# Performance work log

Measured on AMD Instinct MI355X. Metric: run time of the kernel, lower is better.

Reference implementation:

```python
import jax, jax.numpy as jnp
import numpy as np
from jax import lax

DG = 8  # deformable groups


def conv3(x, w, b):
    # 3x3 stride-1 SAME conv, NCHW/OIHW
    y = lax.conv_general_dilated(x, w, (1, 1), 'SAME',
                                 dimension_numbers=('NCHW', 'OIHW', 'NCHW'))
    return y + b[None, :, None, None]


def lrelu(x):
    return jnp.where(x >= 0, x, 0.1 * x)


def _mdcn(x, offset, mask, w, b, dg):
    """Modulated deformable conv v2: 3x3, stride 1, pad 1, dilation 1, groups 1.
    offset: [B, 2*dg*9, H, W] (first dg*9 = y offsets, second dg*9 = x offsets),
    mask:   [B, dg*9, H, W] (already sigmoided)."""
    B, C, H, W = x.shape
    kk = 9
    Cg = C // dg
    off = offset.reshape(B, 2, dg, kk, H, W)
    oy, ox = off[:, 0], off[:, 1]            # [B, dg, kk, H, W]
    m = mask.reshape(B, dg, kk, H, W)
    ky = (jnp.arange(kk) // 3 - 1).astype(x.dtype).reshape(1, 1, kk, 1, 1)
    kx = (jnp.arange(kk) % 3 - 1).astype(x.dtype).reshape(1, 1, kk, 1, 1)
    hg = jnp.arange(H, dtype=x.dtype).reshape(1, 1, 1, H, 1)
    wg = jnp.arange(W, dtype=x.dtype).reshape(1, 1, 1, 1, W)
    py = hg + ky + oy                        # sampling positions (pad=1 cancels k-1 shift)
    px = wg + kx + ox
    y0 = jnp.floor(py)
    x0 = jnp.floor(px)
    wy = py - y0
    wx = px - x0
    xg = x.reshape(B, dg, Cg, H * W)
    acc = jnp.zeros((B, dg, Cg, kk, H, W), x.dtype)
    for dy, dx, wgt in ((0.0, 0.0, (1 - wy) * (1 - wx)),
                        (0.0, 1.0, (1 - wy) * wx),
                        (1.0, 0.0, wy * (1 - wx)),
                        (1.0, 1.0, wy * wx)):
        yy = y0 + dy
        xx = x0 + dx
        valid = (yy >= 0) & (yy < H) & (xx >= 0) & (xx < W)
        yi = jnp.clip(yy, 0, H - 1).astype(jnp.int32)
        xi = jnp.clip(xx, 0, W - 1).astype(jnp.int32)
        idx = (yi * W + xi).reshape(B, dg, 1, kk * H * W)
        v = jnp.take_along_axis(xg, idx, axis=3).reshape(B, dg, Cg, kk, H, W)
        acc = acc + v * (wgt * valid.astype(x.dtype))[:, :, None]
    acc = acc * m[:, :, None]                # modulation mask
    sampled = acc.reshape(B, C, kk, H, W)
    out = jnp.einsum('bckhw,ock->bohw', sampled, w.reshape(w.shape[0], C, kk))
    return out + b[None, :, None, None]


def _dcn_pack(x, feat, w_om, b_om, w, b):
    out = conv3(feat, w_om, b_om)            # [B, 3*dg*9, H, W]
    o1, o2, mr = jnp.split(out, 3, axis=1)
    offset = jnp.concatenate([o1, o2], axis=1)
    mask = jax.nn.sigmoid(mr)
    return _mdcn(x, offset, mask, w, b, DG)


def _forward(ref, neb,
             w_oc1, b_oc1, w_om1, b_om1, w_dcn1, b_dcn1, w_fc, b_fc,
             w_cas1, b_cas1, w_cas2, b_cas2, w_om2, b_om2, w_dcn2, b_dcn2,
             w_ta1, b_ta1, w_ta2, b_ta2, w_ff, b_ff):
    start = ref
    # --- PCD alignment (nbr_feat_l = neb, ref_feat_l = ref) ---
    off = lrelu(conv3(jnp.concatenate([neb, ref], axis=1), w_oc1, b_oc1))
    feat = _dcn_pack(neb, off, w_om1, b_om1, w_dcn1, b_dcn1)
    feat = lrelu(conv3(feat, w_fc, b_fc))
    off = jnp.concatenate([feat, ref], axis=1)
    off = lrelu(conv3(lrelu(conv3(off, w_cas1, b_cas1)), w_cas2, b_cas2))
    feat = lrelu(_dcn_pack(feat, off, w_om2, b_om2, w_dcn2, b_dcn2))
    # --- TSA fusion (ref=ref, neb=feat) ---
    emb_ref = conv3(ref, w_ta1, b_ta1)
    emb = conv3(feat, w_ta2, b_ta2)
    corr = jnp.sum(emb * emb_ref, axis=1, keepdims=True)  # [B,1,H,W]
    feat = lrelu(conv3(ref * corr, w_ff, b_ff))
    return feat + start


def setup_inputs() -> dict:
    key = jax.random.key(0)
    ks = jax.random.split(key, 32)
    B, C, H, W = 4, 64, 180, 320
    s = 0.05
    p = lambda k, shape: (jax.random.normal(k, shape, jnp.float32) * s)
    OM = 3 * DG * 9  # 216
    return {
        'ref': jax.random.normal(ks[0], (B, C, H, W), jnp.float32),
        'neb': jax.random.normal(ks[1], (B, C, H, W), jnp.float32),
        'w_oc1': p(ks[2], (C, 2 * C, 3, 3)), 'b_oc1': p(ks[3], (C,)),
        'w_om1': p(ks[4], (OM, C, 3, 3)),    'b_om1': p(ks[5], (OM,)),
        'w_dcn1': p(ks[6], (C, C, 3, 3)),    'b_dcn1': p(ks[7], (C,)),
        'w_fc': p(ks[8], (C, C, 3, 3)),      'b_fc': p(ks[9], (C,)),
        'w_cas1': p(ks[10], (C, 2 * C, 3, 3)), 'b_cas1': p(ks[11], (C,)),
        'w_cas2': p(ks[12], (C, C, 3, 3)),   'b_cas2': p(ks[13], (C,)),
        'w_om2': p(ks[14], (OM, C, 3, 3)),   'b_om2': p(ks[15], (OM,)),
        'w_dcn2': p(ks[16], (C, C, 3, 3)),   'b_dcn2': p(ks[17], (C,)),
        'w_ta1': p(ks[18], (C, C, 3, 3)),    'b_ta1': p(ks[19], (C,)),
        'w_ta2': p(ks[20], (C, C, 3, 3)),    'b_ta2': p(ks[21], (C,)),
        'w_ff': p(ks[22], (C, C, 3, 3)),     'b_ff': p(ks[23], (C,)),
    }


def reference(ref, neb,
              w_oc1, b_oc1, w_om1, b_om1, w_dcn1, b_dcn1, w_fc, b_fc,
              w_cas1, b_cas1, w_cas2, b_cas2, w_om2, b_om2, w_dcn2, b_dcn2,
              w_ta1, b_ta1, w_ta2, b_ta2, w_ff, b_ff):
    return _forward(ref, neb,
                    w_oc1, b_oc1, w_om1, b_om1, w_dcn1, b_dcn1, w_fc, b_fc,
                    w_cas1, b_cas1, w_cas2, b_cas2, w_om2, b_om2, w_dcn2, b_dcn2,
                    w_ta1, b_ta1, w_ta2, b_ta2, w_ff, b_ff)
```

## Files before the change

kernel.cpp:

```cpp
#include <hip/hip_runtime.h>
#include <cmath>


using short8 = __attribute__((ext_vector_type(8))) short;
using f32x4  = __attribute__((ext_vector_type(4))) float;

#define DEVINL static __device__ __forceinline__

DEVINL unsigned short f2bf(float f){
    unsigned u = __float_as_uint(f);
    u += 0x7fffu + ((u >> 16) & 1u);
    return (unsigned short)(u >> 16);
}
DEVINL unsigned pack2(float a, float b){ return (unsigned)f2bf(a) | ((unsigned)f2bf(b) << 16); }
DEVINL float bflo(unsigned u){ return __uint_as_float(u << 16); }
DEVINL float bfhi(unsigned u){ return __uint_as_float(u & 0xffff0000u); }
DEVINL float bf2f(unsigned short u){ return __uint_as_float((unsigned)u << 16); }
DEVINL float lrelu_f(float v){ return v >= 0.f ? v : 0.1f * v; }

__global__ __launch_bounds__(256) void nchw2nhwc(const float* __restrict__ in,
                                                 unsigned short* __restrict__ out)
{
    constexpr int HW = 180 * 320;
    size_t idx = (size_t)blockIdx.x * 256 + threadIdx.x;
    size_t bb = idx / HW, p = idx % HW;
    const float* src = in + (bb * 64) * (size_t)HW + p;
    unsigned short* dst = out + idx * 64;
    #pragma unroll
    for (int c0 = 0; c0 < 64; c0 += 16) {
        unsigned r[8];
        #pragma unroll
        for (int q = 0; q < 8; ++q)
            r[q] = pack2(src[(size_t)(c0 + 2*q) * HW], src[(size_t)(c0 + 2*q + 1) * HW]);
        *(uint4*)(dst + c0)     = *(uint4*)&r[0];
        *(uint4*)(dst + c0 + 8) = *(uint4*)&r[4];
    }
}

__global__ __launch_bounds__(256) void prep_conv_w(const float* __restrict__ w,
                                                   unsigned short* __restrict__ dst,
                                                   int COUT, int CIN, int total)
{
    int idx = blockIdx.x * 256 + threadIdx.x;
    if (idx >= total) return;
    int ncs = CIN / 32;
    int kk = idx & 31, oc_l = (idx >> 5) & 63, rest = idx >> 11;
    int cs = rest % ncs; int rest2 = rest / ncs;
    int j = rest2 % 9; int ch = rest2 / 9;
    int oc = ch * 64 + oc_l, c = cs * 32 + kk;
    float v = (oc < COUT) ? w[((size_t)oc * CIN + c) * 9 + j] : 0.f;
    dst[idx] = f2bf(v);
}

__global__ __launch_bounds__(256) void prep_dcn_w(const float* __restrict__ w,
                                                  unsigned short* __restrict__ dst)
{
    int idx = blockIdx.x * 256 + threadIdx.x;
    int kk = idx & 31, oc = (idx >> 5) & 63, s = idx >> 11;
    int k = s * 32 + kk;
    int gt = k >> 3, c8 = k & 7;
    int g = gt / 9, tp = gt - g * 9;
    dst[idx] = f2bf(w[((size_t)oc * 64 + g * 8 + c8) * 9 + tp]);
}

template<int CIN, bool TWO_IN, bool ACT, bool SCALE, int OUTMODE>
__global__ __launch_bounds__(256, (CIN == 128 ? 2 : 3)) void conv_mfma(
    const unsigned short* __restrict__ in0, const unsigned short* __restrict__ in1,
    const unsigned short* __restrict__ wgt, const float* __restrict__ bias,
    unsigned short* __restrict__ out, const float* __restrict__ corr,
    const float* __restrict__ res, float* __restrict__ outf, int COUT)
{
    constexpr int H = 180, W = 320, HW = H * W;
    constexpr int NCB = CIN / 8;
    constexpr int NCS = CIN / 32;
    __shared__ __align__(16) unsigned char lds[6 * 34 * CIN * 2];

    const int tid = threadIdx.x;
    const int b  = (OUTMODE == 1) ? 0 : blockIdx.z;
    const int ch = (OUTMODE == 1) ? blockIdx.z : 0;
    const int x0 = blockIdx.x * 32, y0 = blockIdx.y * 4;

    for (int t = tid; t < 6 * 34 * NCB; t += 256) {
        int cb = t % NCB; int r = t / NCB;
        int xp = r % 34, yp = r / 34;
        int gx = x0 - 1 + xp, gy = y0 - 1 + yp;
        uint4 v = make_uint4(0, 0, 0, 0);
        if (gx >= 0 && gx < W && gy >= 0 && gy < H) {
            size_t pix = (size_t)b * HW + (size_t)gy * W + gx;
            const unsigned short* src;
            if (TWO_IN) src = (cb < 8) ? (in0 + pix * 64 + cb * 8) : (in1 + pix * 64 + (cb - 8) * 8);
            else        src = in0 + pix * CIN + cb * 8;
            v = *(const uint4*)src;
            if (SCALE) {
                float cv = corr[pix];
                v.x = pack2(bflo(v.x) * cv, bfhi(v.x) * cv);
                v.y = pack2(bflo(v.y) * cv, bfhi(v.y) * cv);
                v.z = pack2(bflo(v.z) * cv, bfhi(v.z) * cv);
                v.w = pack2(bflo(v.w) * cv, bfhi(v.w) * cv);
            }
        }
        int blk = cb ^ (xp & 7);
        *(uint4*)&lds[(size_t)((yp * 34 + xp) * NCB + blk) * 16] = v;
    }
    __syncthreads();

    const int wv = tid >> 6, lane = tid & 63;
    const int ll = lane & 15, lh = lane >> 4;
    const unsigned short* wchunk = wgt + (size_t)ch * (9 * NCS * 2048);
    const int alane = ll * 32 + lh * 8;

    f32x4 acc[4][2];
    #pragma unroll
    for (int mi = 0; mi < 4; ++mi)
        #pragma unroll
        for (int nf = 0; nf < 2; ++nf) acc[mi][nf] = f32x4{0.f, 0.f, 0.f, 0.f};

    #pragma unroll
    for (int j = 0; j < 9; ++j) {
        const int jy = j / 3, jx = j % 3;
        #pragma unroll
        for (int cs = 0; cs < NCS; ++cs) {
            const int s = j * NCS + cs;
            short8 a[4];
            #pragma unroll
            for (int mi = 0; mi < 4; ++mi)
                a[mi] = *(const short8*)(wchunk + (size_t)s * 2048 + mi * 512 + alane);
            short8 bf[2];
            #pragma unroll
            for (int nf = 0; nf < 2; ++nf) {
                int xp = nf * 16 + ll + jx;
                int blk = (cs * 4 + lh) ^ (xp & 7);
                int addr = (((wv + jy) * 34 + xp) * NCB + blk) * 16;
                bf[nf] = *(const short8*)&lds[addr];
            }
            #pragma unroll
            for (int mi = 0; mi < 4; ++mi)
                #pragma unroll
                for (int nf = 0; nf < 2; ++nf)
                    acc[mi][nf] = __builtin_amdgcn_mfma_f32_16x16x32_bf16(a[mi], bf[nf], acc[mi][nf], 0, 0, 0);
        }
    }

    const int py = y0 + wv;
    const size_t pixrow = (size_t)b * HW + (size_t)py * W;
    #pragma unroll
    for (int nf = 0; nf < 2; ++nf) {
        const int px = x0 + nf * 16 + ll;
        if (OUTMODE == 3) {
            float dot = 0.f;
            const unsigned* er = (const unsigned*)(in1 + (pixrow + px) * 64);
            #pragma unroll
            for (int mi = 0; mi < 4; ++mi) {
                const int oc_l = mi * 16 + lh * 4;
                unsigned e0 = er[oc_l / 2], e1 = er[oc_l / 2 + 1];
                float t0 = acc[mi][nf][0] + bias[oc_l + 0];
                float t1 = acc[mi][nf][1] + bias[oc_l + 1];
                float t2 = acc[mi][nf][2] + bias[oc_l + 2];
                float t3 = acc[mi][nf][3] + bias[oc_l + 3];
                dot += t0 * bflo(e0) + t1 * bfhi(e0) + t2 * bflo(e1) + t3 * bfhi(e1);
            }
            dot += __shfl_xor(dot, 16);
            dot += __shfl_xor(dot, 32);
            if (lh == 0) outf[pixrow + px] = dot;
        } else {
            #pragma unroll
            for (int mi = 0; mi < 4; ++mi) {
                const int oc_l = mi * 16 + lh * 4;
                if (OUTMODE == 0) {
                    float v[4];
                    #pragma unroll
                    for (int jj = 0; jj < 4; ++jj) {
                        float t = acc[mi][nf][jj] + bias[oc_l + jj];
                        v[jj] = ACT ? lrelu_f(t) : t;
                    }
                    uint2 st; st.x = pack2(v[0], v[1]); st.y = pack2(v[2], v[3]);
                    *(uint2*)&out[(pixrow + px) * 64 + oc_l] = st;
                } else if (OUTMODE == 1) {
                    #pragma unroll
                    for (int jj = 0; jj < 4; ++jj) {
                        int ocg = ch * 64 + oc_l + jj;
                        if (ocg < COUT) {
                            float t = acc[mi][nf][jj] + bias[ocg];
                            out[(size_t)ocg * HW + (size_t)py * W + px] = f2bf(ACT ? lrelu_f(t) : t);
                        }
                    }
                } else {
                    #pragma unroll
                    for (int jj = 0; jj < 4; ++jj) {
                        int oc = oc_l + jj;
                        float t = acc[mi][nf][jj] + bias[oc];
                        if (ACT) t = lrelu_f(t);
                        size_t idx = ((size_t)b * 64 + oc) * HW + (size_t)py * W + px;
                        outf[idx] = t + res[idx];
                    }
                }
            }
        }
    }
}

template<int ACT>
__global__ __launch_bounds__(256, 8) void mdcn_mfma(
    const unsigned short* __restrict__ x, size_t xstride,
    const unsigned short* __restrict__ om, size_t omstride,
    const unsigned short* __restrict__ wgt, const float* __restrict__ bias,
    unsigned short* __restrict__ out, size_t ostride)
{
    constexpr int H = 180, W = 320, HW = H * W;
    __shared__ __align__(16) unsigned char sv[36 * 32 * 16];

    const int tid = threadIdx.x;
    const unsigned short* xb  = x  + (size_t)blockIdx.z * xstride;
    const unsigned short* omb = om + (size_t)blockIdx.z * omstride;
    unsigned short* ob        = out + (size_t)blockIdx.z * ostride;
    const int px0 = blockIdx.x * 32;
    const int py  = blockIdx.y;

    const int wv = tid >> 6, lane = tid & 63;
    const int ll = lane & 15, lh = lane >> 4;
    f32x4 acc[2] = {f32x4{0.f,0.f,0.f,0.f}, f32x4{0.f,0.f,0.f,0.f}};

    const int pxl = tid & 31, gg = (tid >> 5) & 3, rep = tid >> 7;
    const int px = px0 + pxl;
    const size_t p = (size_t)py * W + px;
    const int k_begin = rep ? 5 : 0, k_end = rep ? 9 : 5;

    #pragma unroll
    for (int h = 0; h < 2; ++h) {
        const int g = h * 4 + gg;
        for (int k = k_begin; k < k_end; ++k) {
            float oy = bf2f(omb[(size_t)(g * 9 + k) * HW + p]);
            float ox = bf2f(omb[(size_t)(72 + g * 9 + k) * HW + p]);
            float mr = bf2f(omb[(size_t)(144 + g * 9 + k) * HW + p]);
            float m = 1.f / (1.f + __expf(-mr));
            float pyf = (float)(py + (k / 3) - 1) + oy;
            float pxf = (float)(px + (k % 3) - 1) + ox;
            float y0f = floorf(pyf), x0f = floorf(pxf);
            float wy = pyf - y0f, wx = pxf - x0f;
            int yi = (int)y0f, xi = (int)x0f;
            bool vy0 = (yi >= 0) && (yi < H);
            bool vy1 = (yi + 1 >= 0) && (yi + 1 < H);
            bool vx0 = (xi >= 0) && (xi < W);
            bool vx1 = (xi + 1 >= 0) && (xi + 1 < W);
            float w00 = (vy0 && vx0) ? (1.f - wy) * (1.f - wx) * m : 0.f;
            float w01 = (vy0 && vx1) ? (1.f - wy) * wx * m : 0.f;
            float w10 = (vy1 && vx0) ? wy * (1.f - wx) * m : 0.f;
            float w11 = (vy1 && vx1) ? wy * wx * m : 0.f;
            int yc0 = min(max(yi, 0), H - 1), yc1 = min(max(yi + 1, 0), H - 1);
            int xc0 = min(max(xi, 0), W - 1), xc1 = min(max(xi + 1, 0), W - 1);
            uint4 c00 = *(const uint4*)(xb + ((size_t)(yc0 * W + xc0) * 64 + g * 8));
            uint4 c01 = *(const uint4*)(xb + ((size_t)(yc0 * W + xc1) * 64 + g * 8));
            uint4 c10 = *(const uint4*)(xb + ((size_t)(yc1 * W + xc0) * 64 + g * 8));
            uint4 c11 = *(const uint4*)(xb + ((size_t)(yc1 * W + xc1) * 64 + g * 8));
            const unsigned* p00 = (const unsigned*)&c00;
            const unsigned* p01 = (const unsigned*)&c01;
            const unsigned* p10 = (const unsigned*)&c10;
            const unsigned* p11 = (const unsigned*)&c11;
            unsigned r[4];
            #pragma unroll
            for (int q = 0; q < 4; ++q) {
                float lo = w00 * bflo(p00[q]) + w01 * bflo(p01[q]) + w10 * bflo(p10[q]) + w11 * bflo(p11[q]);
                float hi = w00 * bfhi(p00[q]) + w01 * bfhi(p01[q]) + w10 * bfhi(p10[q]) + w11 * bfhi(p11[q]);
                r[q] = pack2(lo, hi);
            }
            *(uint4*)&sv[(size_t)((gg * 9 + k) * 32 + pxl) * 16] = *(uint4*)r;
        }
        __syncthreads();
        #pragma unroll
        for (int s = 0; s < 9; ++s) {
            short8 a = *(const short8*)(wgt + (size_t)((h * 9 + s) * 64 + wv * 16 + ll) * 32 + lh * 8);
            #pragma unroll
            for (int nf = 0; nf < 2; ++nf) {
                short8 bb = *(const short8*)&sv[(size_t)s * 2048 + lh * 512 + (nf * 16 + ll) * 16];
                acc[nf] = __builtin_amdgcn_mfma_f32_16x16x32_bf16(a, bb, acc[nf], 0, 0, 0);
            }
        }
        __syncthreads();
    }

    #pragma unroll
    for (int nf = 0; nf < 2; ++nf) {
        int opx = px0 + nf * 16 + ll;
        int oc0 = wv * 16 + lh * 4;
        float v[4];
        #pragma unroll
        for (int jj = 0; jj < 4; ++jj) {
            float t = acc[nf][jj] + bias[oc0 + jj];
            v[jj] = ACT ? lrelu_f(t) : t;
        }
        uint2 st; st.x = pack2(v[0], v[1]); st.y = pack2(v[2], v[3]);
        *(uint2*)&ob[((size_t)py * W + opx) * 64 + oc0] = st;
    }
}

extern "C" void kernel_launch(void* const* d_in, const int* in_sizes, int n_in,
                              void* d_out, int out_size, void* d_ws, size_t ws_size,
                              hipStream_t stream)
{
    const float* ref    = (const float*)d_in[0];
    const float* neb    = (const float*)d_in[1];
    const float* w_oc1  = (const float*)d_in[2];  const float* b_oc1  = (const float*)d_in[3];
    const float* w_om1  = (const float*)d_in[4];  const float* b_om1  = (const float*)d_in[5];
    const float* w_dcn1 = (const float*)d_in[6];  const float* b_dcn1 = (const float*)d_in[7];
    const float* w_fc   = (const float*)d_in[8];  const float* b_fc   = (const float*)d_in[9];
    const float* w_cas1 = (const float*)d_in[10]; const float* b_cas1 = (const float*)d_in[11];
    const float* w_cas2 = (const float*)d_in[12]; const float* b_cas2 = (const float*)d_in[13];
    const float* w_om2  = (const float*)d_in[14]; const float* b_om2  = (const float*)d_in[15];
    const float* w_dcn2 = (const float*)d_in[16]; const float* b_dcn2 = (const float*)d_in[17];
    const float* w_ta1  = (const float*)d_in[18]; const float* b_ta1  = (const float*)d_in[19];
    const float* w_ta2  = (const float*)d_in[20]; const float* b_ta2  = (const float*)d_in[21];
    const float* w_ff   = (const float*)d_in[22]; const float* b_ff   = (const float*)d_in[23];

    constexpr int H = 180, W = 320, HW = H * W;
    constexpr size_t CHW = (size_t)HW * 64;
    constexpr size_t SLB = 4 * CHW * 2;
    constexpr size_t OMSLOT_EL = (size_t)HW * 216;
    constexpr size_t OMSLOT_B  = OMSLOT_EL * 2;

    char* wsb = (char*)d_ws;
    unsigned short* S0 = (unsigned short*)(wsb);
    unsigned short* S1 = (unsigned short*)(wsb + SLB);
    unsigned short* S2 = (unsigned short*)(wsb + 2 * SLB);
    unsigned short* S3 = (unsigned short*)(wsb + 3 * SLB);
    float* corrf = (float*)S3;
    unsigned short* ffw = (unsigned short*)(wsb + SLB + (2u << 20));

    char* doutb = (char*)d_out;
    unsigned short* omA0 = (unsigned short*)doutb;
    unsigned short* omA1 = omA0 + OMSLOT_EL;
    unsigned short* wb   = (unsigned short*)(doutb + 2 * OMSLOT_B);
    const bool big = ws_size >= 4 * SLB + 2 * OMSLOT_B;
    unsigned short* omB0 = (unsigned short*)(wsb + 4 * SLB);
    unsigned short* omB1 = omB0 + OMSLOT_EL;

    unsigned short* w_oc1p = wb + 0;
    unsigned short* w_om1p = wb + 73728;
    unsigned short* w_dcn1p= wb + 221184;
    unsigned short* w_fcp  = wb + 258048;
    unsigned short* w_cas1p= wb + 294912;
    unsigned short* w_cas2p= wb + 368640;
    unsigned short* w_om2p = wb + 405504;
    unsigned short* w_dcn2p= wb + 552960;
    unsigned short* w_ta1p = wb + 589824;
    unsigned short* w_ta2p = wb + 626688;
    unsigned short* w_ffp  = wb + 663552;

    dim3 blk(256);
    dim3 g4(10, 45, 4);
    dim3 gm(10, 180, 2);

    nchw2nhwc<<<900, blk, 0, stream>>>(ref, S0);
    nchw2nhwc<<<900, blk, 0, stream>>>(neb, S1);
    auto PCW = [&](const float* src, unsigned short* dst, int cout, int cin, int nch){
        int total = nch * 9 * (cin / 32) * 2048;
        prep_conv_w<<<(total + 255) / 256, blk, 0, stream>>>(src, dst, cout, cin, total);
    };
    PCW(w_oc1, w_oc1p, 64, 128, 1);
    PCW(w_om1, w_om1p, 216, 64, 4);
    prep_dcn_w<<<144, blk, 0, stream>>>(w_dcn1, w_dcn1p);
    PCW(w_fc,  w_fcp,  64, 64, 1);
    PCW(w_cas1, w_cas1p, 64, 128, 1);
    PCW(w_cas2, w_cas2p, 64, 64, 1);
    PCW(w_om2, w_om2p, 216, 64, 4);
    prep_dcn_w<<<144, blk, 0, stream>>>(w_dcn2, w_dcn2p);
    PCW(w_ta1, w_ta1p, 64, 64, 1);
    PCW(w_ta2, w_ta2p, 64, 64, 1);
    PCW(w_ff,  w_ffp,  64, 64, 1);

    conv_mfma<128, true, true, false, 0><<<g4, blk, 0, stream>>>(
        S1, S0, w_oc1p, b_oc1, S2, nullptr, nullptr, nullptr, 64);

    auto omconv = [&](const unsigned short* inp, const unsigned short* wp, const float* bp,
                      unsigned short* slot){
        conv_mfma<64, false, false, false, 1><<<g4, blk, 0, stream>>>(
            inp, nullptr, wp, bp, slot, nullptr, nullptr, nullptr, 216);
    };

    if (big) {
        omconv(S2 + 0 * CHW, w_om1p, b_om1, omA0);
        omconv(S2 + 1 * CHW, w_om1p, b_om1, omA1);
        omconv(S2 + 2 * CHW, w_om1p, b_om1, omB0);
        omconv(S2 + 3 * CHW, w_om1p, b_om1, omB1);
        mdcn_mfma<0><<<gm, blk, 0, stream>>>(S1, CHW, omA0, OMSLOT_EL, w_dcn1p, b_dcn1, S3, CHW);
        mdcn_mfma<0><<<gm, blk, 0, stream>>>(S1 + 2 * CHW, CHW, omB0, OMSLOT_EL, w_dcn1p, b_dcn1, S3 + 2 * CHW, CHW);
    } else {
        for (int pp = 0; pp < 2; ++pp) {
            omconv(S2 + (2 * pp) * CHW, w_om1p, b_om1, omA0);
            omconv(S2 + (2 * pp + 1) * CHW, w_om1p, b_om1, omA1);
            mdcn_mfma<0><<<gm, blk, 0, stream>>>(S1 + 2 * pp * CHW, CHW, omA0, OMSLOT_EL,
                                                 w_dcn1p, b_dcn1, S3 + 2 * pp * CHW, CHW);
        }
    }

    conv_mfma<64, false, true, false, 0><<<g4, blk, 0, stream>>>(
        S3, nullptr, w_fcp, b_fc, S2, nullptr, nullptr, nullptr, 64);
    conv_mfma<128, true, true, false, 0><<<g4, blk, 0, stream>>>(
        S2, S0, w_cas1p, b_cas1, S1, nullptr, nullptr, nullptr, 64);
    conv_mfma<64, false, true, false, 0><<<g4, blk, 0, stream>>>(
        S1, nullptr, w_cas2p, b_cas2, S3, nullptr, nullptr, nullptr, 64);

    if (big) {
        omconv(S3 + 0 * CHW, w_om2p, b_om2, omA0);
        omconv(S3 + 1 * CHW, w_om2p, b_om2, omA1);
        omconv(S3 + 2 * CHW, w_om2p, b_om2, omB0);
        omconv(S3 + 3 * CHW, w_om2p, b_om2, omB1);
        mdcn_mfma<1><<<gm, blk, 0, stream>>>(S2, CHW, omA0, OMSLOT_EL, w_dcn2p, b_dcn2, S1, CHW);
        mdcn_mfma<1><<<gm, blk, 0, stream>>>(S2 + 2 * CHW, CHW, omB0, OMSLOT_EL, w_dcn2p, b_dcn2, S1 + 2 * CHW, CHW);
    } else {
        for (int pp = 0; pp < 2; ++pp) {
            omconv(S3 + (2 * pp) * CHW, w_om2p, b_om2, omA0);
            omconv(S3 + (2 * pp + 1) * CHW, w_om2p, b_om2, omA1);
            mdcn_mfma<1><<<gm, blk, 0, stream>>>(S2 + 2 * pp * CHW, CHW, omA0, OMSLOT_EL,
                                                 w_dcn2p, b_dcn2, S1 + 2 * pp * CHW, CHW);
        }
    }

    conv_mfma<64, false, false, false, 0><<<g4, blk, 0, stream>>>(
        S0, nullptr, w_ta1p, b_ta1, S2, nullptr, nullptr, nullptr, 64);
    conv_mfma<64, false, false, false, 3><<<g4, blk, 0, stream>>>(
        S1, S2, w_ta2p, b_ta2, nullptr, nullptr, nullptr, corrf, 64);

    hipMemcpyAsync(ffw, w_ffp, 36864 * 2, hipMemcpyDeviceToDevice, stream);

    conv_mfma<64, false, true, true, 2><<<g4, blk, 0, stream>>>(
        S0, nullptr, ffw, b_ff, nullptr, corrf, ref, (float*)d_out, 64);
}
```

Before: 1.378 ms.

## Batch prep kernels into single launches and restructure MDCN sampling to one pass

Merges the two NCHW-to-NHWC conversions into one launch and the eleven weight-prep kernels into a single 2D-grid launch, cutting kernel launch overhead. The modulated deformable conv kernel now has each thread handle one group across all 9 taps in one pass. Offsets and masks are loaded up front for memory-level parallelism, and the 18 MFMA k-steps run after a single barrier. This doubles LDS per block and lowers the occupancy hint from 8 to 4 blocks per SM, trading occupancy for fewer syncs and more loads in flight.

```diff
diff --git a/kernel.cpp b/kernel.cpp
--- a/kernel.cpp
+++ b/kernel.cpp
@@ -18,11 +18,16 @@
 DEVINL float bf2f(unsigned short u){ return __uint_as_float((unsigned)u << 16); }
 DEVINL float lrelu_f(float v){ return v >= 0.f ? v : 0.1f * v; }
 
-__global__ __launch_bounds__(256) void nchw2nhwc(const float* __restrict__ in,
-                                                 unsigned short* __restrict__ out)
+__global__ __launch_bounds__(256) void nchw2nhwc2(const float* __restrict__ inA,
+                                                  const float* __restrict__ inB,
+                                                  unsigned short* __restrict__ outA,
+                                                  unsigned short* __restrict__ outB)
 {
     constexpr int HW = 180 * 320;
-    size_t idx = (size_t)blockIdx.x * 256 + threadIdx.x;
+    const int blk = blockIdx.x;
+    const float* in = (blk < 900) ? inA : inB;
+    unsigned short* out = (blk < 900) ? outA : outB;
+    size_t idx = (size_t)(blk % 900) * 256 + threadIdx.x;
     size_t bb = idx / HW, p = idx % HW;
     const float* src = in + (bb * 64) * (size_t)HW + p;
     unsigned short* dst = out + idx * 64;
@@ -37,30 +42,35 @@
     }
 }
 
-__global__ __launch_bounds__(256) void prep_conv_w(const float* __restrict__ w,
-                                                   unsigned short* __restrict__ dst,
-                                                   int COUT, int CIN, int total)
+struct PrepArgs {
+    const float* src[11];
+    unsigned short* dst[11];
+    int cout[11]; int cin[11]; int nch[11]; int kind[11];
+};
+
+__global__ __launch_bounds__(256) void prep_all(PrepArgs a)
 {
-    int idx = blockIdx.x * 256 + threadIdx.x;
-    if (idx >= total) return;
-    int ncs = CIN / 32;
-    int kk = idx & 31, oc_l = (idx >> 5) & 63, rest = idx >> 11;
-    int cs = rest % ncs; int rest2 = rest / ncs;
-    int j = rest2 % 9; int ch = rest2 / 9;
-    int oc = ch * 64 + oc_l, c = cs * 32 + kk;
-    float v = (oc < COUT) ? w[((size_t)oc * CIN + c) * 9 + j] : 0.f;
-    dst[idx] = f2bf(v);
-}
-
-__global__ __launch_bounds__(256) void prep_dcn_w(const float* __restrict__ w,
-                                                  unsigned short* __restrict__ dst)
-{
-    int idx = blockIdx.x * 256 + threadIdx.x;
-    int kk = idx & 31, oc = (idx >> 5) & 63, s = idx >> 11;
-    int k = s * 32 + kk;
-    int gt = k >> 3, c8 = k & 7;
-    int g = gt / 9, tp = gt - g * 9;
-    dst[idx] = f2bf(w[((size_t)oc * 64 + g * 8 + c8) * 9 + tp]);
+    const int t = blockIdx.y;
+    const int idx = blockIdx.x * 256 + threadIdx.x;
+    if (a.kind[t] == 1) {
+        if (idx >= 36864) return;
+        int kk = idx & 31, oc = (idx >> 5) & 63, s = idx >> 11;
+        int k = s * 32 + kk;
+        int gt = k >> 3, c8 = k & 7;
+        int g = gt / 9, tp = gt - g * 9;
+        a.dst[t][idx] = f2bf(a.src[t][((size_t)oc * 64 + g * 8 + c8) * 9 + tp]);
+    } else {
+        int cin = a.cin[t], cout = a.cout[t];
+        int ncs = cin / 32;
+        int total = a.nch[t] * 9 * ncs * 2048;
+        if (idx >= total) return;
+        int kk = idx & 31, oc_l = (idx >> 5) & 63, rest = idx >> 11;
+        int cs = rest % ncs; int rest2 = rest / ncs;
+        int j = rest2 % 9; int ch = rest2 / 9;
+        int oc = ch * 64 + oc_l, c = cs * 32 + kk;
+        float v = (oc < cout) ? a.src[t][((size_t)oc * cin + c) * 9 + j] : 0.f;
+        a.dst[t][idx] = f2bf(v);
+    }
 }
 
 template<int CIN, bool TWO_IN, bool ACT, bool SCALE, int OUTMODE>
@@ -200,14 +210,14 @@
 }
 
 template<int ACT>
-__global__ __launch_bounds__(256, 8) void mdcn_mfma(
+__global__ __launch_bounds__(256, 4) void mdcn_mfma(
     const unsigned short* __restrict__ x, size_t xstride,
     const unsigned short* __restrict__ om, size_t omstride,
     const unsigned short* __restrict__ wgt, const float* __restrict__ bias,
     unsigned short* __restrict__ out, size_t ostride)
 {
     constexpr int H = 180, W = 320, HW = H * W;
-    __shared__ __align__(16) unsigned char sv[36 * 32 * 16];
+    __shared__ __align__(16) unsigned char sv[72 * 32 * 16];
 
     const int tid = threadIdx.x;
     const unsigned short* xb  = x  + (size_t)blockIdx.z * xstride;
@@ -216,25 +226,25 @@
     const int px0 = blockIdx.x * 32;
     const int py  = blockIdx.y;
 
-    const int wv = tid >> 6, lane = tid & 63;
-    const int ll = lane & 15, lh = lane >> 4;
-    f32x4 acc[2] = {f32x4{0.f,0.f,0.f,0.f}, f32x4{0.f,0.f,0.f,0.f}};
-
-    const int pxl = tid & 31, gg = (tid >> 5) & 3, rep = tid >> 7;
-    const int px = px0 + pxl;
-    const size_t p = (size_t)py * W + px;
-    const int k_begin = rep ? 5 : 0, k_end = rep ? 9 : 5;
-
-    #pragma unroll
-    for (int h = 0; h < 2; ++h) {
-        const int g = h * 4 + gg;
-        for (int k = k_begin; k < k_end; ++k) {
-            float oy = bf2f(omb[(size_t)(g * 9 + k) * HW + p]);
-            float ox = bf2f(omb[(size_t)(72 + g * 9 + k) * HW + p]);
-            float mr = bf2f(omb[(size_t)(144 + g * 9 + k) * HW + p]);
-            float m = 1.f / (1.f + __expf(-mr));
-            float pyf = (float)(py + (k / 3) - 1) + oy;
-            float pxf = (float)(px + (k % 3) - 1) + ox;
+    {
+        const int pxl = tid & 31, g = tid >> 5;
+        const int px = px0 + pxl;
+        const size_t p = (size_t)py * W + px;
+        const unsigned short* omg = omb + (size_t)(g * 9) * HW + p;
+
+        float oyv[9], oxv[9], mmv[9];
+        #pragma unroll
+        for (int k = 0; k < 9; ++k) oyv[k] = bf2f(omg[(size_t)k * HW]);
+        #pragma unroll
+        for (int k = 0; k < 9; ++k) oxv[k] = bf2f(omg[(size_t)(72 + k) * HW]);
+        #pragma unroll
+        for (int k = 0; k < 9; ++k) mmv[k] = bf2f(omg[(size_t)(144 + k) * HW]);
+
+        #pragma unroll
+        for (int k = 0; k < 9; ++k) {
+            float m = 1.f / (1.f + __expf(-mmv[k]));
+            float pyf = (float)(py + (k / 3) - 1) + oyv[k];
+            float pxf = (float)(px + (k % 3) - 1) + oxv[k];
             float y0f = floorf(pyf), x0f = floorf(pxf);
             float wy = pyf - y0f, wx = pxf - x0f;
             int yi = (int)y0f, xi = (int)x0f;
@@ -263,21 +273,23 @@
                 float hi = w00 * bfhi(p00[q]) + w01 * bfhi(p01[q]) + w10 * bfhi(p10[q]) + w11 * bfhi(p11[q]);
                 r[q] = pack2(lo, hi);
             }
-            *(uint4*)&sv[(size_t)((gg * 9 + k) * 32 + pxl) * 16] = *(uint4*)r;
-        }
-        __syncthreads();
-        #pragma unroll
-        for (int s = 0; s < 9; ++s) {
-            short8 a = *(const short8*)(wgt + (size_t)((h * 9 + s) * 64 + wv * 16 + ll) * 32 + lh * 8);
-            #pragma unroll
-            for (int nf = 0; nf < 2; ++nf) {
-                short8 bb = *(const short8*)&sv[(size_t)s * 2048 + lh * 512 + (nf * 16 + ll) * 16];
-                acc[nf] = __builtin_amdgcn_mfma_f32_16x16x32_bf16(a, bb, acc[nf], 0, 0, 0);
-            }
-        }
-        __syncthreads();
-    }
-
+            *(uint4*)&sv[(size_t)((g * 9 + k) * 32 + pxl) * 16] = *(uint4*)r;
+        }
+    }
+    __syncthreads();
+
+    const int wv = tid >> 6, lane = tid & 63;
+    const int ll = lane & 15, lh = lane >> 4;
+    f32x4 acc[2] = {f32x4{0.f,0.f,0.f,0.f}, f32x4{0.f,0.f,0.f,0.f}};
+    #pragma unroll
+    for (int s = 0; s < 18; ++s) {
+        short8 a = *(const short8*)(wgt + (size_t)(s * 64 + wv * 16 + ll) * 32 + lh * 8);
+        #pragma unroll
+        for (int nf = 0; nf < 2; ++nf) {
+            short8 bb = *(const short8*)&sv[(size_t)s * 2048 + lh * 512 + (nf * 16 + ll) * 16];
+            acc[nf] = __builtin_amdgcn_mfma_f32_16x16x32_bf16(a, bb, acc[nf], 0, 0, 0);
+        }
+    }
     #pragma unroll
     for (int nf = 0; nf < 2; ++nf) {
         int opx = px0 + nf * 16 + ll;
@@ -349,23 +361,22 @@
     dim3 g4(10, 45, 4);
     dim3 gm(10, 180, 2);
 
-    nchw2nhwc<<<900, blk, 0, stream>>>(ref, S0);
-    nchw2nhwc<<<900, blk, 0, stream>>>(neb, S1);
-    auto PCW = [&](const float* src, unsigned short* dst, int cout, int cin, int nch){
-        int total = nch * 9 * (cin / 32) * 2048;
-        prep_conv_w<<<(total + 255) / 256, blk, 0, stream>>>(src, dst, cout, cin, total);
-    };
-    PCW(w_oc1, w_oc1p, 64, 128, 1);
-    PCW(w_om1, w_om1p, 216, 64, 4);
-    prep_dcn_w<<<144, blk, 0, stream>>>(w_dcn1, w_dcn1p);
-    PCW(w_fc,  w_fcp,  64, 64, 1);
-    PCW(w_cas1, w_cas1p, 64, 128, 1);
-    PCW(w_cas2, w_cas2p, 64, 64, 1);
-    PCW(w_om2, w_om2p, 216, 64, 4);
-    prep_dcn_w<<<144, blk, 0, stream>>>(w_dcn2, w_dcn2p);
-    PCW(w_ta1, w_ta1p, 64, 64, 1);
-    PCW(w_ta2, w_ta2p, 64, 64, 1);
-    PCW(w_ff,  w_ffp,  64, 64, 1);
+    nchw2nhwc2<<<1800, blk, 0, stream>>>(ref, neb, S0, S1);
+
+    {
+        PrepArgs pa;
+        const float* srcs[11] = {w_oc1, w_om1, w_dcn1, w_fc, w_cas1, w_cas2, w_om2, w_dcn2, w_ta1, w_ta2, w_ff};
+        unsigned short* dsts[11] = {w_oc1p, w_om1p, w_dcn1p, w_fcp, w_cas1p, w_cas2p, w_om2p, w_dcn2p, w_ta1p, w_ta2p, w_ffp};
+        int couts[11] = {64, 216, 0, 64, 64, 64, 216, 0, 64, 64, 64};
+        int cins[11]  = {128, 64, 0, 64, 128, 64, 64, 0, 64, 64, 64};
+        int nchs[11]  = {1, 4, 0, 1, 1, 1, 4, 0, 1, 1, 1};
+        int kinds[11] = {0, 0, 1, 0, 0, 0, 0, 1, 0, 0, 0};
+        for (int i = 0; i < 11; ++i) {
+            pa.src[i] = srcs[i]; pa.dst[i] = dsts[i];
+            pa.cout[i] = couts[i]; pa.cin[i] = cins[i]; pa.nch[i] = nchs[i]; pa.kind[i] = kinds[i];
+        }
+        prep_all<<<dim3(576, 11), blk, 0, stream>>>(pa);
+    }
 
     conv_mfma<128, true, true, false, 0><<<g4, blk, 0, stream>>>(
         S1, S0, w_oc1p, b_oc1, S2, nullptr, nullptr, nullptr, 64);
```

Result: faster. 1.295 ms (-6.1%).
